# Performance work log

Hardware: AMD Instinct MI355X
Metric: run time of the kernel (lower is better)

The kernel has to match this reference:

```python
import jax, jax.numpy as jnp
import numpy as np

B, T, D = 64, 2048, 64
M_DIM = 8            # pthdv_m
N_GROUPS = 4         # out_dim // m^2 * 4
GD = D // N_GROUPS   # 16, per-group channel dim
OUT_DIM = 64
SE_HID = OUT_DIM // 16  # reduction ratio 16 -> 4


def expm(A):
    """Batched matrix exponential via fixed scaling-and-squaring + Taylor-12.
    A: (..., m, m) with modest norm (skew-symmetric from small weights)."""
    s = 6
    A = A * (1.0 / (2 ** s))
    eye = jnp.eye(A.shape[-1], dtype=A.dtype)
    term = jnp.broadcast_to(eye, A.shape)
    out = term
    for k in range(1, 13):
        term = jnp.matmul(term, A) / k
        out = out + term
    for _ in range(s):
        out = jnp.matmul(out, out)
    return out


def layernorm(x, g, b, eps=1e-5):
    mu = jnp.mean(x, axis=-1, keepdims=True)
    var = jnp.var(x, axis=-1, keepdims=True)
    return (x - mu) * jax.lax.rsqrt(var + eps) * g + b


def lin_interp(f, t_out):
    """F.interpolate(mode='linear', align_corners=False) along axis 1. f: (B,L,C)."""
    L = f.shape[1]
    pos = (jnp.arange(t_out, dtype=f.dtype) + 0.5) * (L / t_out) - 0.5
    pos = jnp.clip(pos, 0.0, L - 1.0)
    i0 = jnp.floor(pos).astype(jnp.int32)
    i1 = jnp.minimum(i0 + 1, L - 1)
    w = (pos - i0.astype(f.dtype))[None, :, None]
    return f[:, i0] * (1.0 - w) + f[:, i1] * w


def setup_inputs() -> dict:
    key = jax.random.key(0)
    ks = jax.random.split(key, 8)
    x = jax.random.normal(ks[0], (B, T, D), dtype=jnp.float32)
    mask = jnp.ones((B, T), dtype=jnp.float32)
    W_dev = jax.random.normal(ks[1], (N_GROUPS, GD, M_DIM, M_DIM), dtype=jnp.float32) * 0.1
    ln_gamma = jnp.ones((M_DIM * M_DIM,), dtype=jnp.float32)
    ln_beta = jnp.zeros((M_DIM * M_DIM,), dtype=jnp.float32)
    cf = N_GROUPS * M_DIM * M_DIM  # 256
    proj_w = jax.random.normal(ks[2], (cf, OUT_DIM), dtype=jnp.float32) / np.sqrt(cf)
    proj_b = jnp.zeros((OUT_DIM,), dtype=jnp.float32)
    se_w1 = jax.random.normal(ks[3], (OUT_DIM, SE_HID), dtype=jnp.float32) / np.sqrt(OUT_DIM)
    se_b1 = jnp.zeros((SE_HID,), dtype=jnp.float32)
    se_w2 = jax.random.normal(ks[4], (SE_HID, OUT_DIM), dtype=jnp.float32) / np.sqrt(SE_HID)
    se_b2 = jnp.zeros((OUT_DIM,), dtype=jnp.float32)
    return {"x": x, "mask": mask, "W_dev": W_dev, "ln_gamma": ln_gamma, "ln_beta": ln_beta,
            "proj_w": proj_w, "proj_b": proj_b, "se_w1": se_w1, "se_b1": se_b1,
            "se_w2": se_w2, "se_b2": se_b2}


def reference(x, mask, W_dev, ln_gamma, ln_beta, proj_w, proj_b, se_w1, se_b1, se_w2, se_b2):
    Bc, Tc, Dc = x.shape
    # skew-symmetric (so(m)) projection of raw dev weights: (G, gd, m, m)
    Wl = jnp.tril(W_dev, k=-1)
    S = Wl - jnp.swapaxes(Wl, -1, -2)
    # grouped increments: (B, T-1, G, gd), masked
    xg = x.reshape(Bc, Tc, N_GROUPS, GD)
    dX = (xg[:, 1:] - xg[:, :-1]) * mask[:, 1:, None, None]
    # project increments to Lie algebra: (B, T', G, m, m)
    Mlie = jnp.einsum('btgd,gdij->btgij', dX, S)
    E = expm(Mlie)                                   # path development per window (kernel=2)
    f = E.reshape(Bc, Tc - 1, N_GROUPS, M_DIM * M_DIM)
    f = layernorm(f, ln_gamma, ln_beta)              # shared LN over m^2, per group
    f = f.reshape(Bc, Tc - 1, N_GROUPS * M_DIM * M_DIM)
    f = f @ proj_w + proj_b                          # (B, T-1, out_dim)
    f = lin_interp(f, Tc)                            # back to length T (stride=1)
    h = x + f
    # Squeeze-and-Excitation with masked average pooling
    denom = jnp.sum(mask, axis=1, keepdims=True)     # (B,1)
    pooled = jnp.sum(h * mask[:, :, None], axis=1) / denom  # (B, D)
    s = jax.nn.sigmoid(jax.nn.gelu(pooled @ se_w1 + se_b1, approximate=False) @ se_w2 + se_b2)
    h = h * s[:, None, :]
    out = h + x                                      # res_con is Identity (in_dim==out_dim, stride==1)
    return (out, mask)
```

## Files before the change

kernel.cpp:

```cpp
#include <hip/hip_runtime.h>

#define B_   64
#define T_   2048
#define TM1  2047
#define D_   64

#define PID(i,j) ((i)*((i)-1)/2 + (j))
#define UID(i,j) ((i)*8 + (j) - (i)*((i)+1)/2)

typedef __attribute__((ext_vector_type(8))) short bf16x8;
typedef __attribute__((ext_vector_type(4))) float f32x4;

__device__ __forceinline__ unsigned f2bf(float v) {
    unsigned u = __float_as_uint(v);
    u = (u + 0x7FFFu + ((u >> 16) & 1u)) >> 16;
    return u;
}
__device__ __forceinline__ float bf2f(unsigned s) {
    return __uint_as_float(s << 16);
}

__global__ void k_prep(const float* __restrict__ pw, unsigned short* __restrict__ pwB,
                       float* __restrict__ pooled)
{
    int idx = blockIdx.x * 256 + threadIdx.x;
    int j  = idx & 7;
    int l  = (idx >> 3) & 63;
    int ks = (idx >> 9) & 7;
    int nt = idx >> 12;
    int k  = ks * 32 + ((l >> 4) << 3) + j;
    int o  = nt * 16 + (l & 15);
    pwB[idx] = (unsigned short)f2bf(pw[k * 64 + o]);
    if (idx < 4160) pooled[idx] = 0.f;
}

__global__ __launch_bounds__(256, 3) void k_expm_f3(
    const float* __restrict__ x, const float* __restrict__ mask,
    const float* __restrict__ Wd, const float* __restrict__ lng,
    const float* __restrict__ lnb, const unsigned short* __restrict__ pwB,
    const float* __restrict__ pb, unsigned short* __restrict__ fbf,
    float* __restrict__ pooled, float* __restrict__ denom)
{
    __shared__ __align__(16) unsigned char smem[32768];
    float* xT = (float*)smem;

    const int tid  = threadIdx.x;
    const int lane = tid & 63;
    const int wq   = __builtin_amdgcn_readfirstlane(tid >> 6);
    const int bl   = blockIdx.x >> 5;
    const int t0   = (blockIdx.x & 31) << 6;

    const float* xb = x + (size_t)bl * (T_ * D_);
    for (int idx = tid; idx < 65 * 64; idx += 256) {
        int r = idx >> 6, c = idx & 63;
        int tr = t0 + r;
        xT[c * 65 + r] = (tr < T_) ? xb[tr * 64 + c] : 0.f;
    }
    __syncthreads();

    const int t = t0 + lane;
    const bool valid = (t < TM1);
    const float* mrow = mask + bl * T_;
    const float mk = valid ? mrow[t + 1] : 0.f;

    {
        const int c  = tid & 63;
        const int rg = tid >> 6;
        float psum = 0.f;
        #pragma unroll
        for (int i = 0; i < 16; ++i) {
            int r = rg * 16 + i;
            psum = fmaf(xT[c * 65 + r], mrow[t0 + r], psum);
        }
        atomicAdd(&pooled[bl * 64 + c], psum);
        if (wq == 0) {
            float dv = mrow[t0 + lane];
            #pragma unroll
            for (int off = 32; off >= 1; off >>= 1) dv += __shfl_xor(dv, off);
            if (lane == 0) atomicAdd(&denom[bl], dv);
        }
    }

    float al[28];
    #pragma unroll
    for (int p = 0; p < 28; ++p) al[p] = 0.f;
    const float* Wg = Wd + wq * (16 * 64);
    #pragma unroll
    for (int d = 0; d < 16; ++d) {
        const float* col = &xT[(wq * 16 + d) * 65 + lane];
        float dxd = (col[1] - col[0]) * mk;
        const float* Wrow = Wg + d * 64;
        #pragma unroll
        for (int i = 1; i < 8; ++i)
            #pragma unroll
            for (int j = 0; j < i; ++j)
                al[PID(i, j)] = fmaf(dxd, Wrow[i * 8 + j], al[PID(i, j)]);
    }
    __syncthreads();

    #pragma unroll
    for (int p = 0; p < 28; ++p) al[p] *= 0.125f;

    float Bu[36];
    #pragma unroll
    for (int i = 0; i < 8; ++i)
        #pragma unroll
        for (int j = i; j < 8; ++j) {
            float s = 0.f;
            #pragma unroll
            for (int k = 0; k < 8; ++k) {
                if (k == i || k == j) continue;
                float aki = (k > i) ? al[PID(k, i)] : -al[PID(i, k)];
                float akj = (k > j) ? al[PID(k, j)] : -al[PID(j, k)];
                s = fmaf(aki, akj, s);
            }
            Bu[UID(i, j)] = -s;
        }
    float B2u[36];
    #pragma unroll
    for (int i = 0; i < 8; ++i)
        #pragma unroll
        for (int j = i; j < 8; ++j) {
            float s = 0.f;
            #pragma unroll
            for (int k = 0; k < 8; ++k) {
                int l1 = (i < k) ? i : k, h1 = (i < k) ? k : i;
                int l2 = (k < j) ? k : j, h2 = (k < j) ? j : k;
                s = fmaf(Bu[UID(l1, h1)], Bu[UID(l2, h2)], s);
            }
            B2u[UID(i, j)] = s;
        }
    float B3u[36];
    #pragma unroll
    for (int i = 0; i < 8; ++i)
        #pragma unroll
        for (int j = i; j < 8; ++j) {
            float s = 0.f;
            #pragma unroll
            for (int k = 0; k < 8; ++k) {
                int l1 = (i < k) ? i : k, h1 = (i < k) ? k : i;
                int l2 = (k < j) ? k : j, h2 = (k < j) ? j : k;
                s = fmaf(Bu[UID(l1, h1)], B2u[UID(l2, h2)], s);
            }
            B3u[UID(i, j)] = s;
        }
    #pragma unroll
    for (int i = 0; i < 8; ++i)
        #pragma unroll
        for (int j = i; j < 8; ++j) {
            int id = UID(i, j);
            float b = Bu[id], b2 = B2u[id], b3 = B3u[id];
            float idm = (i == j) ? 1.f : 0.f;
            Bu[id]  = fmaf(b3, 1.f/720.f,  fmaf(b2, 1.f/24.f,  fmaf(b, 0.5f,     idm)));
            B2u[id] = fmaf(b3, 1.f/5040.f, fmaf(b2, 1.f/120.f, fmaf(b, 1.f/6.f,  idm)));
        }
    float R[64];
    #pragma unroll
    for (int i = 0; i < 8; ++i)
        #pragma unroll
        for (int j = 0; j < 8; ++j) {
            int lo = (i < j) ? i : j, hi = (i < j) ? j : i;
            float s = Bu[UID(lo, hi)];
            #pragma unroll
            for (int k = 0; k < 8; ++k) {
                if (k == i) continue;
                float aik = (i > k) ? al[PID(i, k)] : -al[PID(k, i)];
                int l2 = (k < j) ? k : j, h2 = (k < j) ? j : k;
                s = fmaf(aik, B2u[UID(l2, h2)], s);
            }
            R[i * 8 + j] = s;
        }
    for (int sq = 0; sq < 3; ++sq) {
        float nw[64];
        #pragma unroll
        for (int i = 0; i < 8; ++i)
            #pragma unroll
            for (int j = 0; j < 8; ++j) {
                float s = 0.f;
                #pragma unroll
                for (int kk = 0; kk < 8; ++kk)
                    s = fmaf(R[i * 8 + kk], R[kk * 8 + j], s);
                nw[i * 8 + j] = s;
            }
        #pragma unroll
        for (int e = 0; e < 64; ++e) R[e] = nw[e];
    }

    float sum = 0.f, ssq = 0.f;
    #pragma unroll
    for (int e = 0; e < 64; ++e) { sum += R[e]; ssq = fmaf(R[e], R[e], ssq); }
    float mu   = sum * (1.f / 64.f);
    float var  = ssq * (1.f / 64.f) - mu * mu;
    float rstd = rsqrtf(var + 1e-5f);

    #pragma unroll
    for (int eq = 0; eq < 16; ++eq) {
        int e = eq * 4;
        float v0 = fmaf((R[e]   - mu) * rstd, lng[e],   lnb[e]);
        float v1 = fmaf((R[e+1] - mu) * rstd, lng[e+1], lnb[e+1]);
        float v2 = fmaf((R[e+2] - mu) * rstd, lng[e+2], lnb[e+2]);
        float v3 = fmaf((R[e+3] - mu) * rstd, lng[e+3], lnb[e+3]);
        uint2 pk = make_uint2(f2bf(v0) | (f2bf(v1) << 16), f2bf(v2) | (f2bf(v3) << 16));
        int slot = wq * 16 + eq;
        int sw = slot ^ ((lane & 7) << 1);
        *(uint2*)(smem + lane * 512 + sw * 8) = pk;
    }
    __syncthreads();

    f32x4 acc[4];
    #pragma unroll
    for (int nt = 0; nt < 4; ++nt) acc[nt] = (f32x4)(0.f);
    const int arow = wq * 16 + (lane & 15);
    #pragma unroll
    for (int ks = 0; ks < 8; ++ks) {
        int c = ks * 4 + (lane >> 4);
        bf16x8 a = *(const bf16x8*)(smem + arow * 512 + (c ^ (arow & 7)) * 16);
        #pragma unroll
        for (int nt = 0; nt < 4; ++nt) {
            bf16x8 bb = *(const bf16x8*)(pwB + (((nt * 8 + ks) * 64 + lane) << 3));
            acc[nt] = __builtin_amdgcn_mfma_f32_16x16x32_bf16(a, bb, acc[nt], 0, 0, 0);
        }
    }
    __syncthreads();

    unsigned short* fosh = (unsigned short*)smem;
    float bias[4];
    #pragma unroll
    for (int nt = 0; nt < 4; ++nt) bias[nt] = pb[nt * 16 + (lane & 15)];
    float pf[4] = {0.f, 0.f, 0.f, 0.f};
    #pragma unroll
    for (int r = 0; r < 4; ++r) {
        int pl = wq * 16 + ((lane >> 4) << 2) + r;
        int p  = t0 + pl;
        float g = 0.f;
        if (p < TM1) {
            float mp  = mrow[p];
            float mp1 = mrow[p + 1];
            float wlo = (p + 1.5f) * (1.f / 2048.f);
            float whi = 1.f - (p + 0.5f) * (1.f / 2048.f);
            if (p == 0)          g = mp + mp1 * wlo;
            else if (p == 2046)  g = mp * whi + mp1;
            else                 g = mp * whi + mp1 * wlo;
        }
        #pragma unroll
        for (int nt = 0; nt < 4; ++nt) {
            float fv = acc[nt][r] + bias[nt];
            pf[nt] = fmaf(g, fv, pf[nt]);
            fosh[pl * 64 + nt * 16 + (lane & 15)] = (unsigned short)f2bf(fv);
        }
    }
    #pragma unroll
    for (int nt = 0; nt < 4; ++nt) {
        pf[nt] += __shfl_xor(pf[nt], 16);
        pf[nt] += __shfl_xor(pf[nt], 32);
    }
    if (lane < 16) {
        #pragma unroll
        for (int nt = 0; nt < 4; ++nt)
            atomicAdd(&pooled[bl * 64 + nt * 16 + lane], pf[nt]);
    }
    __syncthreads();

    #pragma unroll
    for (int i = 0; i < 2; ++i) {
        int C = i * 256 + tid;
        int row = C >> 3, c = C & 7;
        int p = t0 + row;
        if (p < TM1) {
            uint4 vv = *(const uint4*)(smem + C * 16);
            *(uint4*)(fbf + ((size_t)bl * TM1 + p) * 64 + c * 8) = vv;
        }
    }
}

__global__ void k_apply2(const float* __restrict__ x, const unsigned short* __restrict__ fbf,
                         const float* __restrict__ pooled, const float* __restrict__ denom,
                         const float* __restrict__ mask,
                         const float* __restrict__ w1, const float* __restrict__ b1,
                         const float* __restrict__ w2, const float* __restrict__ b2,
                         float* __restrict__ out, float* __restrict__ out_mask)
{
    __shared__ __align__(16) float sgate[64];
    const int b  = blockIdx.x >> 5;
    const int t0 = (blockIdx.x & 31) << 6;
    const int tid = threadIdx.x;

    if (tid < 64) {
        float p = pooled[b * 64 + tid] / denom[b];
        float hp0 = p * w1[tid * 4 + 0];
        float hp1 = p * w1[tid * 4 + 1];
        float hp2 = p * w1[tid * 4 + 2];
        float hp3 = p * w1[tid * 4 + 3];
        #pragma unroll
        for (int off = 32; off >= 1; off >>= 1) {
            hp0 += __shfl_xor(hp0, off);
            hp1 += __shfl_xor(hp1, off);
            hp2 += __shfl_xor(hp2, off);
            hp3 += __shfl_xor(hp3, off);
        }
        float h0 = hp0 + b1[0], h1 = hp1 + b1[1], h2 = hp2 + b1[2], h3 = hp3 + b1[3];
        h0 = 0.5f * h0 * (1.f + erff(h0 * 0.70710678118654752f));
        h1 = 0.5f * h1 * (1.f + erff(h1 * 0.70710678118654752f));
        h2 = 0.5f * h2 * (1.f + erff(h2 * 0.70710678118654752f));
        h3 = 0.5f * h3 * (1.f + erff(h3 * 0.70710678118654752f));
        float sv = b2[tid];
        sv = fmaf(h0, w2[0 * 64 + tid], sv);
        sv = fmaf(h1, w2[1 * 64 + tid], sv);
        sv = fmaf(h2, w2[2 * 64 + tid], sv);
        sv = fmaf(h3, w2[3 * 64 + tid], sv);
        sgate[tid] = 1.f / (1.f + expf(-sv));
        out_mask[b * T_ + t0 + tid] = mask[b * T_ + t0 + tid];
    }
    __syncthreads();

    const unsigned short* fb = fbf + (size_t)b * (TM1 * 64);
    #pragma unroll
    for (int r = 0; r < 4; ++r) {
        int u  = r * 256 + tid;
        int t  = t0 + (u >> 4);
        int o4 = (u & 15) << 2;
        float pos = fminf(fmaxf((t + 0.5f) * (2047.f / 2048.f) - 0.5f, 0.f), 2046.f);
        int   i0  = (int)pos;
        float w   = pos - (float)i0;
        int   i1  = min(i0 + 1, 2046);
        uint2 u0 = *(const uint2*)(fb + i0 * 64 + o4);
        uint2 u1 = *(const uint2*)(fb + i1 * 64 + o4);
        size_t base = ((size_t)b * T_ + t) * 64 + o4;
        float4 xv = *(const float4*)(x + base);
        float4 sv = *(const float4*)(&sgate[o4]);
        float4 ov;
        float f00 = bf2f(u0.x & 0xffffu), f01 = bf2f(u0.x >> 16);
        float f02 = bf2f(u0.y & 0xffffu), f03 = bf2f(u0.y >> 16);
        float f10 = bf2f(u1.x & 0xffffu), f11 = bf2f(u1.x >> 16);
        float f12 = bf2f(u1.y & 0xffffu), f13 = bf2f(u1.y >> 16);
        ov.x = fmaf(xv.x + f00 * (1.f - w) + f10 * w, sv.x, xv.x);
        ov.y = fmaf(xv.y + f01 * (1.f - w) + f11 * w, sv.y, xv.y);
        ov.z = fmaf(xv.z + f02 * (1.f - w) + f12 * w, sv.z, xv.z);
        ov.w = fmaf(xv.w + f03 * (1.f - w) + f13 * w, sv.w, xv.w);
        *(float4*)(out + base) = ov;
    }
}

extern "C" void kernel_launch(void* const* d_in, const int* in_sizes, int n_in,
                              void* d_out, int out_size, void* d_ws, size_t ws_size,
                              hipStream_t stream)
{
    const float* x    = (const float*)d_in[0];
    const float* mask = (const float*)d_in[1];
    const float* Wd   = (const float*)d_in[2];
    const float* lng  = (const float*)d_in[3];
    const float* lnb  = (const float*)d_in[4];
    const float* pw   = (const float*)d_in[5];
    const float* pb   = (const float*)d_in[6];
    const float* sw1  = (const float*)d_in[7];
    const float* sb1  = (const float*)d_in[8];
    const float* sw2  = (const float*)d_in[9];
    const float* sb2  = (const float*)d_in[10];

    float* out      = (float*)d_out;
    float* out_mask = out + (size_t)B_ * T_ * D_;
    float* pooled = (float*)d_ws;
    float* denom  = pooled + 4096;
    unsigned short* pwB = (unsigned short*)(denom + 64);
    unsigned short* fbf = pwB + 16384;

    hipLaunchKernelGGL(k_prep, dim3(64), dim3(256), 0, stream, pw, pwB, pooled);
    hipLaunchKernelGGL(k_expm_f3, dim3(2048), dim3(256), 0, stream,
                       x, mask, Wd, lng, lnb, pwB, pb, fbf, pooled, denom);
    hipLaunchKernelGGL(k_apply2, dim3(2048), dim3(256), 0, stream,
                       x, fbf, pooled, denom, mask, sw1, sb1, sw2, sb2, out, out_mask);
}
```

Measured before the change: 197.5 us.

## Use cheaper Taylor evaluation with extra squaring, split apply kernel finer, nontemporal IO

The expm kernel now scales the skew matrix by 1/16 instead of 1/8 and drops the A^6 (B3) product, evaluating a lower-order series through a rearranged polynomial. It then performs four squarings instead of three. This trades one symmetric 8x8 product for one full 8x8 squaring while keeping accuracy through the smaller scaled norm. The apply kernel now launches twice as many blocks, each covering half as many timesteps, and uses nontemporal loads and stores for x and the output.

```diff
diff --git a/kernel.cpp b/kernel.cpp
--- a/kernel.cpp
+++ b/kernel.cpp
@@ -34,7 +34,7 @@
     if (idx < 4160) pooled[idx] = 0.f;
 }
 
-__global__ __launch_bounds__(256, 3) void k_expm_f3(
+__global__ __launch_bounds__(256, 3) void k_expm_f4(
     const float* __restrict__ x, const float* __restrict__ mask,
     const float* __restrict__ Wd, const float* __restrict__ lng,
     const float* __restrict__ lnb, const unsigned short* __restrict__ pwB,
@@ -99,7 +99,7 @@
     __syncthreads();
 
     #pragma unroll
-    for (int p = 0; p < 28; ++p) al[p] *= 0.125f;
+    for (int p = 0; p < 28; ++p) al[p] *= 0.0625f;
 
     float Bu[36];
     #pragma unroll
@@ -116,7 +116,7 @@
             }
             Bu[UID(i, j)] = -s;
         }
-    float B2u[36];
+    float c1u[36];
     #pragma unroll
     for (int i = 0; i < 8; ++i)
         #pragma unroll
@@ -128,37 +128,22 @@
                 int l2 = (k < j) ? k : j, h2 = (k < j) ? j : k;
                 s = fmaf(Bu[UID(l1, h1)], Bu[UID(l2, h2)], s);
             }
-            B2u[UID(i, j)] = s;
-        }
-    float B3u[36];
-    #pragma unroll
-    for (int i = 0; i < 8; ++i)
-        #pragma unroll
-        for (int j = i; j < 8; ++j) {
-            float s = 0.f;
-            #pragma unroll
-            for (int k = 0; k < 8; ++k) {
-                int l1 = (i < k) ? i : k, h1 = (i < k) ? k : i;
-                int l2 = (k < j) ? k : j, h2 = (k < j) ? j : k;
-                s = fmaf(Bu[UID(l1, h1)], B2u[UID(l2, h2)], s);
-            }
-            B3u[UID(i, j)] = s;
+            float idm = (i == j) ? 1.f : 0.f;
+            c1u[UID(i, j)] = fmaf(s, 1.f / 120.f, fmaf(Bu[UID(i, j)], 1.f / 6.f, idm));
         }
     #pragma unroll
     for (int i = 0; i < 8; ++i)
         #pragma unroll
         for (int j = i; j < 8; ++j) {
             int id = UID(i, j);
-            float b = Bu[id], b2 = B2u[id], b3 = B3u[id];
-            float idm = (i == j) ? 1.f : 0.f;
-            Bu[id]  = fmaf(b3, 1.f/720.f,  fmaf(b2, 1.f/24.f,  fmaf(b, 0.5f,     idm)));
-            B2u[id] = fmaf(b3, 1.f/5040.f, fmaf(b2, 1.f/120.f, fmaf(b, 1.f/6.f,  idm)));
+            float idm = (i == j) ? 4.f : 0.f;
+            Bu[id] = fmaf(c1u[id], 5.f, -idm) - Bu[id] * (1.f / 3.f);
         }
     float R[64];
     #pragma unroll
-    for (int i = 0; i < 8; ++i)
-        #pragma unroll
-        for (int j = 0; j < 8; ++j) {
+    for (int j = 0; j < 8; ++j)
+        #pragma unroll
+        for (int i = 0; i < 8; ++i) {
             int lo = (i < j) ? i : j, hi = (i < j) ? j : i;
             float s = Bu[UID(lo, hi)];
             #pragma unroll
@@ -166,11 +151,11 @@
                 if (k == i) continue;
                 float aik = (i > k) ? al[PID(i, k)] : -al[PID(k, i)];
                 int l2 = (k < j) ? k : j, h2 = (k < j) ? j : k;
-                s = fmaf(aik, B2u[UID(l2, h2)], s);
+                s = fmaf(aik, c1u[UID(l2, h2)], s);
             }
             R[i * 8 + j] = s;
         }
-    for (int sq = 0; sq < 3; ++sq) {
+    for (int sq = 0; sq < 4; ++sq) {
         float nw[64];
         #pragma unroll
         for (int i = 0; i < 8; ++i)
@@ -281,8 +266,8 @@
                          float* __restrict__ out, float* __restrict__ out_mask)
 {
     __shared__ __align__(16) float sgate[64];
-    const int b  = blockIdx.x >> 5;
-    const int t0 = (blockIdx.x & 31) << 6;
+    const int b  = blockIdx.x >> 6;
+    const int t0 = (blockIdx.x & 63) << 5;
     const int tid = threadIdx.x;
 
     if (tid < 64) {
@@ -309,13 +294,13 @@
         sv = fmaf(h2, w2[2 * 64 + tid], sv);
         sv = fmaf(h3, w2[3 * 64 + tid], sv);
         sgate[tid] = 1.f / (1.f + expf(-sv));
-        out_mask[b * T_ + t0 + tid] = mask[b * T_ + t0 + tid];
-    }
+    }
+    if (tid < 32) out_mask[b * T_ + t0 + tid] = mask[b * T_ + t0 + tid];
     __syncthreads();
 
     const unsigned short* fb = fbf + (size_t)b * (TM1 * 64);
     #pragma unroll
-    for (int r = 0; r < 4; ++r) {
+    for (int r = 0; r < 2; ++r) {
         int u  = r * 256 + tid;
         int t  = t0 + (u >> 4);
         int o4 = (u & 15) << 2;
@@ -326,9 +311,9 @@
         uint2 u0 = *(const uint2*)(fb + i0 * 64 + o4);
         uint2 u1 = *(const uint2*)(fb + i1 * 64 + o4);
         size_t base = ((size_t)b * T_ + t) * 64 + o4;
-        float4 xv = *(const float4*)(x + base);
-        float4 sv = *(const float4*)(&sgate[o4]);
-        float4 ov;
+        f32x4 xv = __builtin_nontemporal_load((const f32x4*)(x + base));
+        f32x4 sv = *(const f32x4*)(&sgate[o4]);
+        f32x4 ov;
         float f00 = bf2f(u0.x & 0xffffu), f01 = bf2f(u0.x >> 16);
         float f02 = bf2f(u0.y & 0xffffu), f03 = bf2f(u0.y >> 16);
         float f10 = bf2f(u1.x & 0xffffu), f11 = bf2f(u1.x >> 16);
@@ -337,7 +322,7 @@
         ov.y = fmaf(xv.y + f01 * (1.f - w) + f11 * w, sv.y, xv.y);
         ov.z = fmaf(xv.z + f02 * (1.f - w) + f12 * w, sv.z, xv.z);
         ov.w = fmaf(xv.w + f03 * (1.f - w) + f13 * w, sv.w, xv.w);
-        *(float4*)(out + base) = ov;
+        __builtin_nontemporal_store(ov, (f32x4*)(out + base));
     }
 }
 
@@ -365,8 +350,8 @@
     unsigned short* fbf = pwB + 16384;
 
     hipLaunchKernelGGL(k_prep, dim3(64), dim3(256), 0, stream, pw, pwB, pooled);
-    hipLaunchKernelGGL(k_expm_f3, dim3(2048), dim3(256), 0, stream,
+    hipLaunchKernelGGL(k_expm_f4, dim3(2048), dim3(256), 0, stream,
                        x, mask, Wd, lng, lnb, pwB, pb, fbf, pooled, denom);
-    hipLaunchKernelGGL(k_apply2, dim3(2048), dim3(256), 0, stream,
+    hipLaunchKernelGGL(k_apply2, dim3(4096), dim3(256), 0, stream,
                        x, fbf, pooled, denom, mask, sw1, sb1, sw2, sb2, out, out_mask);
 }
```

Result: faster. 189.1 us (-4.3%).
